# Kernel tuning notes

Measured on AMD Instinct MI355X. Metric: run time of the kernel, lower is better.

The kernel has to match this reference:

```python
import jax, jax.numpy as jnp
import numpy as np
import math

FIRE_THRESH = 0.85
NUDGE_RATE = 2.0
SQRT_2_OVER_PI = 0.7978845608028654
EPS_NORM = 1e-12


def _gelu(x):
    return 0.5 * x * (1.0 + jnp.tanh(SQRT_2_OVER_PI * (x + 0.044715 * x * x * x)))


def setup_inputs() -> dict:
    key = jax.random.key(0)
    k1, k2, k3, k4, k5 = jax.random.split(key, 5)
    B, T, D, N = 4, 2048, 2048, 512
    x = jax.random.normal(k1, (B, T, D), dtype=jnp.float32)
    buf = jax.random.normal(k2, (N, D), dtype=jnp.float32)
    xbuf = jax.random.normal(k3, (N, D), dtype=jnp.float32)
    inj = jax.random.uniform(k4, (N,), dtype=jnp.float32)
    xglobal = jax.random.normal(k5, (D,), dtype=jnp.float32)
    mask = jnp.ones((N,), dtype=bool)
    log_inject = jnp.asarray(math.log(0.1), dtype=jnp.float32)
    return {"x": x, "log_inject": log_inject, "buf": buf, "xbuf": xbuf,
            "inj": inj, "xglobal": xglobal, "mask": mask}


def reference(x, log_inject, buf, xbuf, inj, xglobal, mask):
    B, T, D = x.shape
    sg = jax.lax.stop_gradient

    inject_base = jnp.clip(jnp.exp(log_inject), 0.001, 2.0)
    y_plain = _gelu(x)
    # detached batch-mean of the plain GELU output, [D]
    y_mean = sg(jnp.mean(y_plain.reshape(B * T, D), axis=0))

    # masked cosine similarity lookup against buffer, [N]
    m_n = y_mean / jnp.maximum(jnp.linalg.norm(y_mean), EPS_NORM)
    buf_n = buf / jnp.maximum(jnp.linalg.norm(buf, axis=-1, keepdims=True), EPS_NORM)
    sims = jnp.where(mask, buf_n @ m_n, -1.0)
    nearest_idx = jnp.argmax(sims)
    max_sim = sims[nearest_idx]

    # data-dependent injection-level update (all detached in torch)
    inj_near = inj[nearest_idx]
    fired = max_sim > FIRE_THRESH
    inj_level = jnp.where(fired,
                          jnp.where(inj_near < 1e-6, inject_base, inj_near * NUDGE_RATE),
                          inj_near)
    inj_level = sg(inj_level)
    stored_x = sg(xbuf[nearest_idx])  # [D]

    # nudge direction toward stored prototype, away from global mean
    nudge_dir = stored_x - sg(xglobal)
    nudge_unit = nudge_dir / jnp.maximum(jnp.linalg.norm(nudge_dir), 1e-6)

    # per-token cosine similarity to stored_x, [B, T] (x detached)
    x_det = sg(x)
    x_n = x_det / jnp.maximum(jnp.linalg.norm(x_det, axis=-1, keepdims=True), EPS_NORM)
    sn_n = stored_x / jnp.maximum(jnp.linalg.norm(stored_x), EPS_NORM)
    tok_sim = jnp.clip(x_n @ sn_n, 0.0, 1.0)  # [B, T]

    x_adj = x + inj_level * tok_sim[..., None] * nudge_unit[None, None, :]
    out_nudged = _gelu(x_adj)
    return jnp.where(inj_level < 1e-6, y_plain, out_nudged)
```

## Files before the change

### kernel.cpp

```cpp
#include <hip/hip_runtime.h>
#include <math.h>

#define D 2048
#define NROWS 8192
#define NBUF 512
#define RC 128
#define ROWS_PER_CHUNK 64
#define K4_ROWS 2

__device__ __forceinline__ float rcpf(float v) { return __builtin_amdgcn_rcpf(v); }

__device__ __forceinline__ float gelu_f(float v) {
    float u = v * (1.0f + 0.044715f * v * v);
    float t = -1.5957691216057308f * u;
    return v * rcpf(1.0f + __expf(t));
}

__global__ __launch_bounds__(256) void k1_colsum(const float* __restrict__ x,
                                                 float* __restrict__ partial) {
    const int cg = blockIdx.x * 256 + threadIdx.x;
    const int r0 = blockIdx.y * ROWS_PER_CHUNK;
    const float4* x4 = (const float4*)x;
    float ax = 0.f, ay = 0.f, az = 0.f, aw = 0.f;
    #pragma unroll 4
    for (int r = 0; r < ROWS_PER_CHUNK; ++r) {
        float4 v = x4[(size_t)(r0 + r) * (D / 4) + cg];
        ax += gelu_f(v.x); ay += gelu_f(v.y); az += gelu_f(v.z); aw += gelu_f(v.w);
    }
    float4 o; o.x = ax; o.y = ay; o.z = az; o.w = aw;
    ((float4*)partial)[(size_t)blockIdx.y * (D / 4) + cg] = o;
}

__global__ __launch_bounds__(256) void k1b_reduce(const float* __restrict__ partial,
                                                  float* __restrict__ ysum) {
    const int tid = threadIdx.x;
    const int col   = blockIdx.x * 32 + (tid & 31);
    const int slice = tid >> 5;
    const int k0 = slice * (RC / 8);
    float s = 0.f;
    #pragma unroll 16
    for (int k = 0; k < RC / 8; ++k) s += partial[(size_t)(k0 + k) * D + col];
    __shared__ float red[256];
    red[tid] = s;
    __syncthreads();
    if (tid < 32) {
        float t = red[tid];
        #pragma unroll
        for (int j = 1; j < 8; ++j) t += red[j * 32 + tid];
        ysum[blockIdx.x * 32 + tid] = t;
    }
}

__global__ __launch_bounds__(256) void k2_sims(const float* __restrict__ buf,
                                               const float* __restrict__ xbuf,
                                               const float* __restrict__ xglobal,
                                               const float* __restrict__ ysum,
                                               float* __restrict__ dotv,
                                               float* __restrict__ bn2,
                                               float* __restrict__ xn2,
                                               float* __restrict__ nd2,
                                               float* __restrict__ yn2) {
    const int tid = threadIdx.x;
    const int b = blockIdx.x;
    float dacc = 0.f, nacc = 0.f, xacc = 0.f, ndacc = 0.f;
    const float4* y4 = (const float4*)ysum;
    if (b < NBUF) {
        const float4* b4 = (const float4*)(buf + (size_t)b * D);
        const float4* s4 = (const float4*)(xbuf + (size_t)b * D);
        const float4* g4 = (const float4*)xglobal;
        #pragma unroll
        for (int c = tid; c < D / 4; c += 256) {
            float4 bv = b4[c]; float4 yv = y4[c];
            float4 sv = s4[c]; float4 gv = g4[c];
            dacc += bv.x * yv.x + bv.y * yv.y + bv.z * yv.z + bv.w * yv.w;
            nacc += bv.x * bv.x + bv.y * bv.y + bv.z * bv.z + bv.w * bv.w;
            xacc += sv.x * sv.x + sv.y * sv.y + sv.z * sv.z + sv.w * sv.w;
            float nx = sv.x - gv.x, ny = sv.y - gv.y, nz = sv.z - gv.z, nw = sv.w - gv.w;
            ndacc += nx * nx + ny * ny + nz * nz + nw * nw;
        }
    } else {
        #pragma unroll
        for (int c = tid; c < D / 4; c += 256) {
            float4 yv = y4[c];
            dacc += yv.x * yv.x + yv.y * yv.y + yv.z * yv.z + yv.w * yv.w;
        }
    }
    #pragma unroll
    for (int off = 32; off; off >>= 1) {
        dacc  += __shfl_down(dacc,  off, 64);
        nacc  += __shfl_down(nacc,  off, 64);
        xacc  += __shfl_down(xacc,  off, 64);
        ndacc += __shfl_down(ndacc, off, 64);
    }
    __shared__ float sa[4], sb[4], sc[4], sd[4];
    const int lane = tid & 63, w = tid >> 6;
    if (lane == 0) { sa[w] = dacc; sb[w] = nacc; sc[w] = xacc; sd[w] = ndacc; }
    __syncthreads();
    if (tid == 0) {
        float dt = sa[0] + sa[1] + sa[2] + sa[3];
        float nt = sb[0] + sb[1] + sb[2] + sb[3];
        float xt = sc[0] + sc[1] + sc[2] + sc[3];
        float nd = sd[0] + sd[1] + sd[2] + sd[3];
        if (b < NBUF) { dotv[b] = dt; bn2[b] = nt; xn2[b] = xt; nd2[b] = nd; }
        else yn2[0] = dt;
    }
}

__global__ __launch_bounds__(256) void k4_out(const float* __restrict__ x,
                                              const float* __restrict__ xbuf,
                                              const float* __restrict__ xglobal,
                                              const float* __restrict__ dotv,
                                              const float* __restrict__ bn2,
                                              const float* __restrict__ xn2,
                                              const float* __restrict__ nd2,
                                              const float* __restrict__ yn2,
                                              const int* __restrict__ mask,
                                              const float* __restrict__ inj,
                                              const float* __restrict__ log_inject,
                                              float* __restrict__ out) {
    const int tid = threadIdx.x;
    const int lane = tid & 63, w = tid >> 6;
    const size_t row0 = (size_t)blockIdx.x * K4_ROWS;

    __shared__ float sv[4]; __shared__ int si[4];
    __shared__ int s_idx;
    __shared__ float s_lvl, s_rnudge, s_rstored;
    {
        const float rnm = rcpf(fmaxf(sqrtf(yn2[0]) * (1.0f / 8192.0f), 1e-12f));
        float bv; int bi;
        {
            const int i = tid;
            float nb = fmaxf(sqrtf(bn2[i]), 1e-12f);
            float sim = (dotv[i] * (1.0f / 8192.0f)) * rnm * rcpf(nb);
            if (!mask[i]) sim = -1.0f;
            bv = sim; bi = i;
        }
        {
            const int i = tid + 256;
            float nb = fmaxf(sqrtf(bn2[i]), 1e-12f);
            float sim = (dotv[i] * (1.0f / 8192.0f)) * rnm * rcpf(nb);
            if (!mask[i]) sim = -1.0f;
            if (sim > bv) { bv = sim; bi = i; }
        }
        #pragma unroll
        for (int off = 32; off; off >>= 1) {
            float ov = __shfl_down(bv, off, 64);
            int   oi = __shfl_down(bi, off, 64);
            if (ov > bv || (ov == bv && oi < bi)) { bv = ov; bi = oi; }
        }
        if (lane == 0) { sv[w] = bv; si[w] = bi; }
        __syncthreads();
        if (tid == 0) {
            float fv = sv[0]; int fi = si[0];
            #pragma unroll
            for (int j = 1; j < 4; ++j) {
                if (sv[j] > fv || (sv[j] == fv && si[j] < fi)) { fv = sv[j]; fi = si[j]; }
            }
            float ib = fminf(fmaxf(__expf(log_inject[0]), 0.001f), 2.0f);
            float inear = inj[fi];
            s_lvl = (fv > 0.85f) ? ((inear < 1e-6f) ? ib : inear * 2.0f) : inear;
            s_idx = fi;
            s_rnudge  = rcpf(fmaxf(sqrtf(nd2[fi]), 1e-6f));
            s_rstored = rcpf(fmaxf(sqrtf(xn2[fi]), 1e-12f));
        }
        __syncthreads();
    }
    const int   idx       = s_idx;
    const float inj_level = s_lvl;
    const float rnudge    = s_rnudge;
    const float rstored   = s_rstored;

    const float4* sr = (const float4*)(xbuf + (size_t)idx * D);
    const float4* gr = (const float4*)xglobal;
    const float4 s0 = sr[tid], s1 = sr[tid + 256];
    const float4 g0 = gr[tid], g1 = gr[tid + 256];

    const float4* xra = (const float4*)(x + row0 * D);
    const float4* xrb = (const float4*)(x + (row0 + 1) * D);
    const float4 a0 = xra[tid], a1 = xra[tid + 256];
    const float4 b0 = xrb[tid], b1 = xrb[tid + 256];

    float das = a0.x * s0.x + a0.y * s0.y + a0.z * s0.z + a0.w * s0.w
              + a1.x * s1.x + a1.y * s1.y + a1.z * s1.z + a1.w * s1.w;
    float dax = a0.x * a0.x + a0.y * a0.y + a0.z * a0.z + a0.w * a0.w
              + a1.x * a1.x + a1.y * a1.y + a1.z * a1.z + a1.w * a1.w;
    float dbs = b0.x * s0.x + b0.y * s0.y + b0.z * s0.z + b0.w * s0.w
              + b1.x * s1.x + b1.y * s1.y + b1.z * s1.z + b1.w * s1.w;
    float dbx = b0.x * b0.x + b0.y * b0.y + b0.z * b0.z + b0.w * b0.w
              + b1.x * b1.x + b1.y * b1.y + b1.z * b1.z + b1.w * b1.w;

    #pragma unroll
    for (int off = 32; off; off >>= 1) {
        das += __shfl_down(das, off, 64);
        dax += __shfl_down(dax, off, 64);
        dbs += __shfl_down(dbs, off, 64);
        dbx += __shfl_down(dbx, off, 64);
    }
    __shared__ float sas[4], sax[4], sbs[4], sbx[4];
    if (lane == 0) { sas[w] = das; sax[w] = dax; sbs[w] = dbs; sbx[w] = dbx; }
    __syncthreads();
    __shared__ float s_ca, s_cb;
    if (tid == 0) {
        float dta = sas[0] + sas[1] + sas[2] + sas[3];
        float nta = sax[0] + sax[1] + sax[2] + sax[3];
        float rxa = rcpf(fmaxf(sqrtf(nta), 1e-12f));
        float tsa = fminf(fmaxf(dta * rxa * rstored, 0.0f), 1.0f);
        s_ca = (inj_level < 1e-6f) ? 0.0f : inj_level * tsa * rnudge;
        float dtb = sbs[0] + sbs[1] + sbs[2] + sbs[3];
        float ntb = sbx[0] + sbx[1] + sbx[2] + sbx[3];
        float rxb = rcpf(fmaxf(sqrtf(ntb), 1e-12f));
        float tsb = fminf(fmaxf(dtb * rxb * rstored, 0.0f), 1.0f);
        s_cb = (inj_level < 1e-6f) ? 0.0f : inj_level * tsb * rnudge;
    }
    __syncthreads();
    const float ca = s_ca, cb = s_cb;

    float4 o0, o1;
    o0.x = gelu_f(a0.x + ca * (s0.x - g0.x));
    o0.y = gelu_f(a0.y + ca * (s0.y - g0.y));
    o0.z = gelu_f(a0.z + ca * (s0.z - g0.z));
    o0.w = gelu_f(a0.w + ca * (s0.w - g0.w));
    o1.x = gelu_f(a1.x + ca * (s1.x - g1.x));
    o1.y = gelu_f(a1.y + ca * (s1.y - g1.y));
    o1.z = gelu_f(a1.z + ca * (s1.z - g1.z));
    o1.w = gelu_f(a1.w + ca * (s1.w - g1.w));
    float4* orowa = (float4*)(out + row0 * D);
    orowa[tid] = o0; orowa[tid + 256] = o1;

    o0.x = gelu_f(b0.x + cb * (s0.x - g0.x));
    o0.y = gelu_f(b0.y + cb * (s0.y - g0.y));
    o0.z = gelu_f(b0.z + cb * (s0.z - g0.z));
    o0.w = gelu_f(b0.w + cb * (s0.w - g0.w));
    o1.x = gelu_f(b1.x + cb * (s1.x - g1.x));
    o1.y = gelu_f(b1.y + cb * (s1.y - g1.y));
    o1.z = gelu_f(b1.z + cb * (s1.z - g1.z));
    o1.w = gelu_f(b1.w + cb * (s1.w - g1.w));
    float4* orowb = (float4*)(out + (row0 + 1) * D);
    orowb[tid] = o0; orowb[tid + 256] = o1;
}

extern "C" void kernel_launch(void* const* d_in, const int* in_sizes, int n_in,
                              void* d_out, int out_size, void* d_ws, size_t ws_size,
                              hipStream_t stream) {
    const float* x          = (const float*)d_in[0];
    const float* log_inject = (const float*)d_in[1];
    const float* buf        = (const float*)d_in[2];
    const float* xbuf       = (const float*)d_in[3];
    const float* inj        = (const float*)d_in[4];
    const float* xglobal    = (const float*)d_in[5];
    const int*   mask       = (const int*)d_in[6];
    float* out = (float*)d_out;
    float* ws  = (float*)d_ws;

    float* ysum    = ws;
    float* dotv    = ws + 2048;
    float* bn2     = ws + 2560;
    float* xn2     = ws + 3072;
    float* nd2     = ws + 3584;
    float* yn2     = ws + 4088;
    float* partial = ws + 4096;

    k1_colsum<<<dim3(2, RC), 256, 0, stream>>>(x, partial);
    k1b_reduce<<<64, 256, 0, stream>>>(partial, ysum);
    k2_sims<<<NBUF + 1, 256, 0, stream>>>(buf, xbuf, xglobal, ysum,
                                          dotv, bn2, xn2, nd2, yn2);
    k4_out<<<NROWS / K4_ROWS, 256, 0, stream>>>(x, xbuf, xglobal, dotv, bn2,
                                                xn2, nd2, yn2, mask, inj,
                                                log_inject, out);
}
```

Measured before the change: 46.70 us.

## Process eight rows per block in output kernel, re-read x, nontemporal stores

The output kernel now handles eight rows per block instead of two. This spreads the per-block argmax over the 512 buffer similarities and the stored-row loads across more rows. It computes the dot products in a first pass, then re-reads x from cache/L2 in a second pass rather than keeping all rows in registers, and writes the output with nontemporal stores. Chunk sizes for the column-sum stage also change (more, smaller chunks), and the unroll factors are adjusted. The x re-read adds memory traffic if it misses in cache, and fewer blocks reduce parallelism.

```diff
diff --git a/kernel.cpp b/kernel.cpp
--- a/kernel.cpp
+++ b/kernel.cpp
@@ -4,9 +4,11 @@
 #define D 2048
 #define NROWS 8192
 #define NBUF 512
-#define RC 128
-#define ROWS_PER_CHUNK 64
-#define K4_ROWS 2
+#define RC 256
+#define ROWS_PER_CHUNK 32
+#define K4_ROWS 8
+
+typedef float vf4 __attribute__((ext_vector_type(4)));
 
 __device__ __forceinline__ float rcpf(float v) { return __builtin_amdgcn_rcpf(v); }
 
@@ -14,6 +16,11 @@
     float u = v * (1.0f + 0.044715f * v * v);
     float t = -1.5957691216057308f * u;
     return v * rcpf(1.0f + __expf(t));
+}
+
+__device__ __forceinline__ float dot8(float4 p0, float4 p1, float4 q0, float4 q1) {
+    return p0.x * q0.x + p0.y * q0.y + p0.z * q0.z + p0.w * q0.w
+         + p1.x * q1.x + p1.y * q1.y + p1.z * q1.z + p1.w * q1.w;
 }
 
 __global__ __launch_bounds__(256) void k1_colsum(const float* __restrict__ x,
@@ -22,7 +29,7 @@
     const int r0 = blockIdx.y * ROWS_PER_CHUNK;
     const float4* x4 = (const float4*)x;
     float ax = 0.f, ay = 0.f, az = 0.f, aw = 0.f;
-    #pragma unroll 4
+    #pragma unroll 8
     for (int r = 0; r < ROWS_PER_CHUNK; ++r) {
         float4 v = x4[(size_t)(r0 + r) * (D / 4) + cg];
         ax += gelu_f(v.x); ay += gelu_f(v.y); az += gelu_f(v.z); aw += gelu_f(v.w);
@@ -38,7 +45,7 @@
     const int slice = tid >> 5;
     const int k0 = slice * (RC / 8);
     float s = 0.f;
-    #pragma unroll 16
+    #pragma unroll 8
     for (int k = 0; k < RC / 8; ++k) s += partial[(size_t)(k0 + k) * D + col];
     __shared__ float red[256];
     red[tid] = s;
@@ -122,6 +129,9 @@
     const int lane = tid & 63, w = tid >> 6;
     const size_t row0 = (size_t)blockIdx.x * K4_ROWS;
 
+    const float4* gr = (const float4*)xglobal;
+    const float4 g0 = gr[tid], g1 = gr[tid + 256];
+
     __shared__ float sv[4]; __shared__ int si[4];
     __shared__ int s_idx;
     __shared__ float s_lvl, s_rnudge, s_rstored;
@@ -171,72 +181,60 @@
     const float rstored   = s_rstored;
 
     const float4* sr = (const float4*)(xbuf + (size_t)idx * D);
-    const float4* gr = (const float4*)xglobal;
     const float4 s0 = sr[tid], s1 = sr[tid + 256];
-    const float4 g0 = gr[tid], g1 = gr[tid + 256];
-
-    const float4* xra = (const float4*)(x + row0 * D);
-    const float4* xrb = (const float4*)(x + (row0 + 1) * D);
-    const float4 a0 = xra[tid], a1 = xra[tid + 256];
-    const float4 b0 = xrb[tid], b1 = xrb[tid + 256];
-
-    float das = a0.x * s0.x + a0.y * s0.y + a0.z * s0.z + a0.w * s0.w
-              + a1.x * s1.x + a1.y * s1.y + a1.z * s1.z + a1.w * s1.w;
-    float dax = a0.x * a0.x + a0.y * a0.y + a0.z * a0.z + a0.w * a0.w
-              + a1.x * a1.x + a1.y * a1.y + a1.z * a1.z + a1.w * a1.w;
-    float dbs = b0.x * s0.x + b0.y * s0.y + b0.z * s0.z + b0.w * s0.w
-              + b1.x * s1.x + b1.y * s1.y + b1.z * s1.z + b1.w * s1.w;
-    float dbx = b0.x * b0.x + b0.y * b0.y + b0.z * b0.z + b0.w * b0.w
-              + b1.x * b1.x + b1.y * b1.y + b1.z * b1.z + b1.w * b1.w;
-
+
+    float as[K4_ROWS], axx[K4_ROWS];
+    #pragma unroll
+    for (int r = 0; r < K4_ROWS; ++r) {
+        const float4* xr = (const float4*)(x + (row0 + r) * D);
+        float4 v0 = xr[tid], v1 = xr[tid + 256];
+        as[r]  = dot8(v0, v1, s0, s1);
+        axx[r] = dot8(v0, v1, v0, v1);
+    }
     #pragma unroll
     for (int off = 32; off; off >>= 1) {
-        das += __shfl_down(das, off, 64);
-        dax += __shfl_down(dax, off, 64);
-        dbs += __shfl_down(dbs, off, 64);
-        dbx += __shfl_down(dbx, off, 64);
-    }
-    __shared__ float sas[4], sax[4], sbs[4], sbx[4];
-    if (lane == 0) { sas[w] = das; sax[w] = dax; sbs[w] = dbs; sbx[w] = dbx; }
-    __syncthreads();
-    __shared__ float s_ca, s_cb;
-    if (tid == 0) {
-        float dta = sas[0] + sas[1] + sas[2] + sas[3];
-        float nta = sax[0] + sax[1] + sax[2] + sax[3];
-        float rxa = rcpf(fmaxf(sqrtf(nta), 1e-12f));
-        float tsa = fminf(fmaxf(dta * rxa * rstored, 0.0f), 1.0f);
-        s_ca = (inj_level < 1e-6f) ? 0.0f : inj_level * tsa * rnudge;
-        float dtb = sbs[0] + sbs[1] + sbs[2] + sbs[3];
-        float ntb = sbx[0] + sbx[1] + sbx[2] + sbx[3];
-        float rxb = rcpf(fmaxf(sqrtf(ntb), 1e-12f));
-        float tsb = fminf(fmaxf(dtb * rxb * rstored, 0.0f), 1.0f);
-        s_cb = (inj_level < 1e-6f) ? 0.0f : inj_level * tsb * rnudge;
-    }
-    __syncthreads();
-    const float ca = s_ca, cb = s_cb;
-
-    float4 o0, o1;
-    o0.x = gelu_f(a0.x + ca * (s0.x - g0.x));
-    o0.y = gelu_f(a0.y + ca * (s0.y - g0.y));
-    o0.z = gelu_f(a0.z + ca * (s0.z - g0.z));
-    o0.w = gelu_f(a0.w + ca * (s0.w - g0.w));
-    o1.x = gelu_f(a1.x + ca * (s1.x - g1.x));
-    o1.y = gelu_f(a1.y + ca * (s1.y - g1.y));
-    o1.z = gelu_f(a1.z + ca * (s1.z - g1.z));
-    o1.w = gelu_f(a1.w + ca * (s1.w - g1.w));
-    float4* orowa = (float4*)(out + row0 * D);
-    orowa[tid] = o0; orowa[tid + 256] = o1;
-
-    o0.x = gelu_f(b0.x + cb * (s0.x - g0.x));
-    o0.y = gelu_f(b0.y + cb * (s0.y - g0.y));
-    o0.z = gelu_f(b0.z + cb * (s0.z - g0.z));
-    o0.w = gelu_f(b0.w + cb * (s0.w - g0.w));
-    o1.x = gelu_f(b1.x + cb * (s1.x - g1.x));
-    o1.y = gelu_f(b1.y + cb * (s1.y - g1.y));
-    o1.z = gelu_f(b1.z + cb * (s1.z - g1.z));
-    o1.w = gelu_f(b1.w + cb * (s1.w - g1.w));
-    float4* orowb = (float4*)(out + (row0 + 1) * D);
-    orowb[tid] = o0; orowb[tid + 256] = o1;
+        #pragma unroll
+        for (int r = 0; r < K4_ROWS; ++r) {
+            as[r]  += __shfl_down(as[r],  off, 64);
+            axx[r] += __shfl_down(axx[r], off, 64);
+        }
+    }
+    __shared__ float redS[K4_ROWS][4], redX[K4_ROWS][4];
+    if (lane == 0) {
+        #pragma unroll
+        for (int r = 0; r < K4_ROWS; ++r) { redS[r][w] = as[r]; redX[r][w] = axx[r]; }
+    }
+    __syncthreads();
+    __shared__ float s_c[K4_ROWS];
+    if (tid < K4_ROWS) {
+        float dt = redS[tid][0] + redS[tid][1] + redS[tid][2] + redS[tid][3];
+        float nt = redX[tid][0] + redX[tid][1] + redX[tid][2] + redX[tid][3];
+        float rx = rcpf(fmaxf(sqrtf(nt), 1e-12f));
+        float ts = fminf(fmaxf(dt * rx * rstored, 0.0f), 1.0f);
+        s_c[tid] = (inj_level < 1e-6f) ? 0.0f : inj_level * ts * rnudge;
+    }
+    __syncthreads();
+
+    float4 f0, f1;
+    f0.x = s0.x - g0.x; f0.y = s0.y - g0.y; f0.z = s0.z - g0.z; f0.w = s0.w - g0.w;
+    f1.x = s1.x - g1.x; f1.y = s1.y - g1.y; f1.z = s1.z - g1.z; f1.w = s1.w - g1.w;
+
+    const float* x2 = x;
+    asm volatile("" : "+r"(x2));
+    #pragma unroll
+    for (int r = 0; r < K4_ROWS; ++r) {
+        const float4* xr = (const float4*)(x2 + (row0 + r) * D);
+        float4 v0 = xr[tid], v1 = xr[tid + 256];
+        const float c = s_c[r];
+        float4 o0, o1;
+        o0.x = gelu_f(v0.x + c * f0.x); o0.y = gelu_f(v0.y + c * f0.y);
+        o0.z = gelu_f(v0.z + c * f0.z); o0.w = gelu_f(v0.w + c * f0.w);
+        o1.x = gelu_f(v1.x + c * f1.x); o1.y = gelu_f(v1.y + c * f1.y);
+        o1.z = gelu_f(v1.z + c * f1.z); o1.w = gelu_f(v1.w + c * f1.w);
+        vf4* op = (vf4*)(out + (row0 + r) * D);
+        __builtin_nontemporal_store(*(vf4*)&o0, op + tid);
+        __builtin_nontemporal_store(*(vf4*)&o1, op + tid + 256);
+    }
 }
 
 extern "C" void kernel_launch(void* const* d_in, const int* in_sizes, int n_in,
```

Result: slower. 55.36 us (+18.5%).
